# Optimization experiments

Hardware: AMD Instinct MI355X
Metric: run time of the kernel (lower is better)

The kernel has to match this reference:

```python
import jax, jax.numpy as jnp
import numpy as np
from jax import lax

B, H, W = 8, 512, 512


def setup_inputs() -> dict:
    key = jax.random.key(0)
    k1, k2, k3, k4, k5 = jax.random.split(key, 5)
    img = jax.random.uniform(k1, (B, 3, H, W), jnp.float32)
    omega = 0.8 + 0.15 * jax.random.uniform(k2, (B, 1), jnp.float32)
    atmospheric_light = 0.5 + 0.5 * jax.random.uniform(k3, (B, 3), jnp.float32)
    L_low = 2.0 * jax.random.uniform(k4, (B, 1), jnp.float32)          # percent in [0,2)
    L_high = 95.0 + 4.0 * jax.random.uniform(k5, (B, 1), jnp.float32)  # percent in [95,99)
    guided_radius = 15  # python int, uniform across batch (original clamps to [1,50])
    return {"img": img, "omega": omega, "atmospheric_light": atmospheric_light,
            "L_low": L_low, "L_high": L_high, "guided_radius": guided_radius}


def _box_filter(x, r):
    # reflect-pad + mean over (2r+1)x(2r+1) window, separable (exactly avg_pool2d on reflect-padded input)
    k = 2 * r + 1
    xp = jnp.pad(x, ((0, 0), (0, 0), (r, r), (r, r)), mode='reflect')
    s = lax.reduce_window(xp, 0.0, lax.add, (1, 1, k, 1), (1, 1, 1, 1), 'VALID')
    s = lax.reduce_window(s, 0.0, lax.add, (1, 1, 1, k), (1, 1, 1, 1), 'VALID')
    return s / (k * k)


def _forward(img, omega, atmospheric_light, L_low, L_high, r):
    eps = 0.5
    Bb, Cc, Hh, Ww = img.shape
    A = atmospheric_light.reshape(Bb, 3, 1, 1)
    # initial transmission: t = 1 - omega * min_c(I/A)
    dark = jnp.min(img / (A + 1e-8), axis=1, keepdims=True)           # (B,1,H,W)
    t0 = 1.0 - omega.reshape(Bb, 1, 1, 1) * dark
    # gradient constraint (weights from t0, applied to shifted copies)
    wx = jnp.exp(-jnp.abs(t0[:, :, :, 1:] - t0[:, :, :, :-1]))
    tx = jnp.concatenate([t0[:, :, :, :1], t0[:, :, :, :-1] * wx], axis=3)
    wy = jnp.exp(-jnp.abs(t0[:, :, 1:, :] - t0[:, :, :-1, :]))
    tg = jnp.concatenate([tx[:, :, :1, :], tx[:, :, :-1, :] * wy], axis=2)
    # guided filter with grayscale guide
    rgb_w = jnp.array([0.299, 0.587, 0.114], dtype=img.dtype).reshape(1, 3, 1, 1)
    gray = jnp.sum(img * rgb_w, axis=1, keepdims=True)                # (B,1,H,W)
    mI = _box_filter(gray, r)
    mp = _box_filter(tg, r)
    mIp = _box_filter(gray * tg, r)
    cov_Ip = mIp - mI * mp
    var_I = _box_filter(gray * gray, r) - mI * mI
    a = cov_Ip / (var_I + eps)
    b = mp - a * mI
    t_final = jnp.clip(_box_filter(a, r) * gray + _box_filter(b, r), 0.1, 1.0)
    # restoration
    J = jnp.clip((img - A) / (t_final + 1e-8) + A, 0.0, 1.0)
    # percentile color stretch (vectorized over B and C)
    n = Hh * Ww
    svals = jnp.sort(J.reshape(Bb, Cc, n), axis=-1)
    li = jnp.clip((L_low / 100.0 * n).astype(jnp.int32), 0, n - 1)    # (B,1)
    hi = jnp.clip((L_high / 100.0 * n).astype(jnp.int32), 0, n - 1)
    p_low = jnp.take_along_axis(svals, jnp.broadcast_to(li[:, :, None], (Bb, Cc, 1)), axis=-1).reshape(Bb, Cc, 1, 1)
    p_high = jnp.take_along_axis(svals, jnp.broadcast_to(hi[:, :, None], (Bb, Cc, 1)), axis=-1).reshape(Bb, Cc, 1, 1)
    out = (jnp.clip(J, p_low, p_high) - p_low) / (p_high - p_low + 1e-8)
    return jnp.clip(out, 0.0, 1.0)


def reference(img, omega, atmospheric_light, L_low, L_high, guided_radius):
    r = max(1, min(int(guided_radius), 50))
    return _forward(img, omega, atmospheric_light, L_low, L_high, r)
```

## Files before the change

kernel.cpp:

```cpp
#include <hip/hip_runtime.h>
#include <cstdint>

constexpr int Bb = 8, Hh = 512, Ww = 512;
constexpr int HWn = Hh * Ww;
constexpr int CH23 = 8;
constexpr int CHK4 = 16;
constexpr int NBIN = 1024;
constexpr int NSUB = 32;

__device__ __forceinline__ int reflect_idx(int p, int n) {
    p = (p < 0) ? -p : p;
    return (p < n) ? p : (2 * n - 2 - p);
}
__device__ __forceinline__ int clamp_r(const int* rad) {
    int r = rad[0];
    return (r < 1) ? 1 : ((r > 50) ? 50 : r);
}

__global__ __launch_bounds__(512) void k1_stats_h(
    const float* __restrict__ img, const float* __restrict__ omega,
    const float* __restrict__ atm, const int* __restrict__ rad,
    float4* __restrict__ hq, unsigned int* __restrict__ histzero)
{
    const int i = blockIdx.x;
    const int b = blockIdx.y;
    const int j = threadIdx.x;
    const int fbid = b * gridDim.x + i;
    if (fbid < 48) histzero[fbid * 512 + j] = 0u;
    const int r = clamp_r(rad);

    __shared__ float t0c[512], t0p[512];
    __shared__ float4 Pb[512];
    __shared__ float4 wsum[8];

    const float om = omega[b];
    const float iA0 = 1.0f / (atm[b*3+0] + 1e-8f);
    const float iA1 = 1.0f / (atm[b*3+1] + 1e-8f);
    const float iA2 = 1.0f / (atm[b*3+2] + 1e-8f);
    const float* imb = img + (size_t)b * 3 * HWn;
    const int ip = (i > 0) ? (i - 1) : 0;

    float r0 = imb[0*HWn + i*Ww + j];
    float g0 = imb[1*HWn + i*Ww + j];
    float b0 = imb[2*HWn + i*Ww + j];
    t0c[j] = 1.0f - om * fminf(fminf(r0*iA0, g0*iA1), b0*iA2);
    float r1 = imb[0*HWn + ip*Ww + j];
    float g1 = imb[1*HWn + ip*Ww + j];
    float b1 = imb[2*HWn + ip*Ww + j];
    t0p[j] = 1.0f - om * fminf(fminf(r1*iA0, g1*iA1), b1*iA2);
    float gr = 0.299f*r0 + 0.587f*g0 + 0.114f*b0;
    __syncthreads();

    float tx = (j == 0) ? t0p[0] : t0p[j-1] * __expf(-fabsf(t0p[j] - t0p[j-1]));
    float tgv = (i == 0) ? tx : tx * __expf(-fabsf(t0c[j] - t0p[j]));

    const int lane = j & 63, wv = j >> 6;
    float4 incl;
    incl.x = gr; incl.y = tgv; incl.z = gr * tgv; incl.w = gr * gr;
    #pragma unroll
    for (int off = 1; off < 64; off <<= 1) {
        float ux = __shfl_up(incl.x, off);
        float uy = __shfl_up(incl.y, off);
        float uz = __shfl_up(incl.z, off);
        float uw = __shfl_up(incl.w, off);
        if (lane >= off) { incl.x += ux; incl.y += uy; incl.z += uz; incl.w += uw; }
    }
    if (lane == 63) wsum[wv] = incl;
    __syncthreads();
    float4 o4; o4.x = 0.f; o4.y = 0.f; o4.z = 0.f; o4.w = 0.f;
    #pragma unroll
    for (int w = 0; w < 7; ++w) {
        if (w < wv) {
            float4 t = wsum[w];
            o4.x += t.x; o4.y += t.y; o4.z += t.z; o4.w += t.w;
        }
    }
    float4 P; P.x = incl.x + o4.x; P.y = incl.y + o4.y; P.z = incl.z + o4.z; P.w = incl.w + o4.w;
    Pb[j] = P;
    __syncthreads();

    const int lo = j - r, hi = j + r;
    float4 s = Pb[(hi > 511) ? 511 : hi];
    if (lo > 0) {
        float4 t = Pb[lo-1];
        s.x -= t.x; s.y -= t.y; s.z -= t.z; s.w -= t.w;
    }
    if (lo < 0) {
        float4 t = Pb[r - j], u = Pb[0];
        s.x += t.x - u.x; s.y += t.y - u.y; s.z += t.z - u.z; s.w += t.w - u.w;
    }
    if (hi > 511) {
        float4 t = Pb[510], u = Pb[1021 - j - r];
        s.x += t.x - u.x; s.y += t.y - u.y; s.z += t.z - u.z; s.w += t.w - u.w;
    }
    hq[((size_t)b * Hh + i) * Ww + j] = s;
}

__global__ __launch_bounds__(512) void k23_ab_h(
    const float4* __restrict__ hq, const int* __restrict__ rad,
    float2* __restrict__ hab)
{
    const int b  = blockIdx.y;
    const int y0 = blockIdx.x * CH23;
    const int j  = threadIdx.x;
    const int r  = clamp_r(rad);
    const float ikk = 1.0f / (float)((2*r+1) * (2*r+1));
    const int lane = j & 63, wv = j >> 6;

    __shared__ float2 Pb[512];
    __shared__ float2 wsum[8];

    float4 s; s.x = 0.f; s.y = 0.f; s.z = 0.f; s.w = 0.f;
    for (int d = -r; d <= r; ++d) {
        int m = reflect_idx(y0 + d, Hh);
        float4 v = hq[((size_t)b * Hh + m) * Ww + j];
        s.x += v.x; s.y += v.y; s.z += v.z; s.w += v.w;
    }

    for (int y = y0; y < y0 + CH23; ++y) {
        float mI = s.x * ikk, mp = s.y * ikk, mIp = s.z * ikk, mII = s.w * ikk;
        float av = (mIp - mI * mp) / (mII - mI * mI + 0.5f);
        float bv = mp - av * mI;

        float2 incl; incl.x = av; incl.y = bv;
        #pragma unroll
        for (int off = 1; off < 64; off <<= 1) {
            float ux = __shfl_up(incl.x, off);
            float uy = __shfl_up(incl.y, off);
            if (lane >= off) { incl.x += ux; incl.y += uy; }
        }
        if (lane == 63) wsum[wv] = incl;
        __syncthreads();
        float ox = 0.f, oy = 0.f;
        #pragma unroll
        for (int w = 0; w < 7; ++w) {
            if (w < wv) { float2 t = wsum[w]; ox += t.x; oy += t.y; }
        }
        float2 P; P.x = incl.x + ox; P.y = incl.y + oy;
        Pb[j] = P;
        __syncthreads();

        const int lo = j - r, hi = j + r;
        float2 hs = Pb[(hi > 511) ? 511 : hi];
        if (lo > 0)   { float2 t = Pb[lo-1];  hs.x -= t.x; hs.y -= t.y; }
        if (lo < 0)   { float2 t = Pb[r-j], u = Pb[0];
                        hs.x += t.x - u.x; hs.y += t.y - u.y; }
        if (hi > 511) { float2 t = Pb[510], u = Pb[1021-j-r];
                        hs.x += t.x - u.x; hs.y += t.y - u.y; }
        hab[((size_t)b * Hh + y) * Ww + j] = hs;

        int yin  = reflect_idx(y + 1 + r, Hh);
        int yout = reflect_idx(y - r, Hh);
        float4 vi = hq[((size_t)b * Hh + yin)  * Ww + j];
        float4 vo = hq[((size_t)b * Hh + yout) * Ww + j];
        s.x += vi.x - vo.x; s.y += vi.y - vo.y; s.z += vi.z - vo.z; s.w += vi.w - vo.w;
    }
}

__global__ __launch_bounds__(256) void k4_final_v(
    const float2* __restrict__ hab, const float* __restrict__ img,
    const float* __restrict__ atm, const int* __restrict__ rad,
    float* __restrict__ J)
{
    const int b  = blockIdx.y;
    const int y0 = blockIdx.x * CHK4;
    const int j  = blockIdx.z * 256 + threadIdx.x;
    const int r  = clamp_r(rad);
    const float ikk = 1.0f / (float)((2*r+1) * (2*r+1));

    float Aa[3];
    Aa[0] = atm[b*3+0]; Aa[1] = atm[b*3+1]; Aa[2] = atm[b*3+2];
    const float* imb = img + (size_t)b * 3 * HWn;
    float* Jb = J + (size_t)b * 3 * HWn;
    const float2* habb = hab + (size_t)b * Hh * Ww + j;

    float2 V; V.x = 0.f; V.y = 0.f;
    for (int d = -r; d <= r; ++d) {
        int m = reflect_idx(y0 + d, Hh);
        float2 v = habb[(size_t)m * Ww];
        V.x += v.x; V.y += v.y;
    }

    #pragma unroll
    for (int g = 0; g < CHK4; g += 4) {
        const int yb = y0 + g;
        float2 vi[4], vo[4];
        float cr[4], cg[4], cb[4];
        #pragma unroll
        for (int q = 0; q < 4; ++q) {
            const int y = yb + q;
            vi[q] = habb[(size_t)reflect_idx(y + 1 + r, Hh) * Ww];
            vo[q] = habb[(size_t)reflect_idx(y - r, Hh) * Ww];
            const size_t po = (size_t)y * Ww + j;
            cr[q] = imb[0*HWn + po];
            cg[q] = imb[1*HWn + po];
            cb[q] = imb[2*HWn + po];
        }
        #pragma unroll
        for (int q = 0; q < 4; ++q) {
            const int y = yb + q;
            const size_t po = (size_t)y * Ww + j;
            float g_ = 0.299f*cr[q] + 0.587f*cg[q] + 0.114f*cb[q];
            float t = fminf(fmaxf((V.x * g_ + V.y) * ikk, 0.1f), 1.0f);
            float invt = 1.0f / (t + 1e-8f);
            Jb[0*HWn + po] = fminf(fmaxf((cr[q] - Aa[0]) * invt + Aa[0], 0.f), 1.f);
            Jb[1*HWn + po] = fminf(fmaxf((cg[q] - Aa[1]) * invt + Aa[1], 0.f), 1.f);
            Jb[2*HWn + po] = fminf(fmaxf((cb[q] - Aa[2]) * invt + Aa[2], 0.f), 1.f);
            V.x += vi[q].x - vo[q].x;
            V.y += vi[q].y - vo[q].y;
        }
    }
}

__global__ __launch_bounds__(256) void k5_hist(
    const float4* __restrict__ J, unsigned int* __restrict__ hist)
{
    const int bc  = blockIdx.x >> 5;
    const int sub = blockIdx.x & (NSUB - 1);
    const int tid = threadIdx.x;
    __shared__ unsigned int lh[NBIN];
    for (int i = tid; i < NBIN; i += 256) lh[i] = 0u;
    __syncthreads();

    const float4* base = J + (size_t)bc * (HWn / 4) + (size_t)sub * (HWn / 4 / NSUB);
    unsigned int clo = 0, chi = 0;
    for (int i = tid; i < HWn / 4 / NSUB; i += 256) {
        float4 v = base[i];
        #pragma unroll
        for (int c = 0; c < 4; ++c) {
            float f = (c == 0) ? v.x : (c == 1) ? v.y : (c == 2) ? v.z : v.w;
            int bin = (int)(f * (float)NBIN);
            bin = (bin > NBIN-1) ? NBIN-1 : bin;
            if (bin == 0)           clo++;
            else if (bin == NBIN-1) chi++;
            else atomicAdd(&lh[bin], 1u);
        }
    }
    if (clo) atomicAdd(&lh[0], clo);
    if (chi) atomicAdd(&lh[NBIN-1], chi);
    __syncthreads();
    for (int i = tid; i < NBIN; i += 256) {
        unsigned int v = lh[i];
        if (v) atomicAdd(&hist[(size_t)bc * NBIN + i], v);
    }
}

__global__ __launch_bounds__(64) void k5_decide(
    const unsigned int* __restrict__ hist,
    const float* __restrict__ L_low, const float* __restrict__ L_high,
    float* __restrict__ p_low, float* __restrict__ p_high)
{
    const int t  = blockIdx.x / 24;
    const int bc = blockIdx.x % 24;
    const int b  = bc / 3;
    const int lane = threadIdx.x;
    const unsigned int* hb = hist + (size_t)bc * NBIN;

    unsigned int loc[NBIN / 64];
    unsigned int lsum = 0;
    #pragma unroll
    for (int i = 0; i < NBIN / 64; ++i) { loc[i] = hb[lane * (NBIN/64) + i]; lsum += loc[i]; }

    unsigned int incl = lsum;
    #pragma unroll
    for (int off = 1; off < 64; off <<= 1) {
        unsigned int v = __shfl_up(incl, off);
        if (lane >= off) incl += v;
    }
    unsigned int excl = incl - lsum;

    float L = t ? L_high[b] : L_low[b];
    int k = (int)(L * (1.0f / 100.0f) * (float)HWn);
    k = (k < 0) ? 0 : ((k > HWn - 1) ? HWn - 1 : k);

    if ((unsigned int)k >= excl && (unsigned int)k < incl) {
        unsigned int c = excl;
        #pragma unroll
        for (int i = 0; i < NBIN / 64; ++i) {
            if ((unsigned int)k < c + loc[i]) {
                float val = ((float)(lane * (NBIN/64) + i) + 0.5f) * (1.0f / (float)NBIN);
                if (t) p_high[bc] = val;
                else   p_low[bc]  = val;
                break;
            }
            c += loc[i];
        }
    }
}

__global__ __launch_bounds__(256) void k6_norm(
    float4* __restrict__ J,
    const float* __restrict__ p_low, const float* __restrict__ p_high)
{
    size_t idx = (size_t)blockIdx.x * 256 + threadIdx.x;
    int bc = (int)(idx >> 16);
    float l = p_low[bc], h = p_high[bc];
    float inv = 1.0f / (h - l + 1e-8f);
    float4 v = J[idx];
    v.x = fminf(fmaxf((fminf(fmaxf(v.x, l), h) - l) * inv, 0.f), 1.f);
    v.y = fminf(fmaxf((fminf(fmaxf(v.y, l), h) - l) * inv, 0.f), 1.f);
    v.z = fminf(fmaxf((fminf(fmaxf(v.z, l), h) - l) * inv, 0.f), 1.f);
    v.w = fminf(fmaxf((fminf(fmaxf(v.w, l), h) - l) * inv, 0.f), 1.f);
    J[idx] = v;
}

extern "C" void kernel_launch(void* const* d_in, const int* in_sizes, int n_in,
                              void* d_out, int out_size, void* d_ws, size_t ws_size,
                              hipStream_t stream)
{
    const float* img    = (const float*)d_in[0];
    const float* omega  = (const float*)d_in[1];
    const float* atm    = (const float*)d_in[2];
    const float* L_low  = (const float*)d_in[3];
    const float* L_high = (const float*)d_in[4];
    const int*   rad    = (const int*)d_in[5];
    float* J  = (float*)d_out;
    float* ws = (float*)d_ws;

    const size_t F = (size_t)Bb * HWn;
    float4* hq  = (float4*)ws;
    float2* hab = (float2*)(ws + 4 * F);
    unsigned int* hist = (unsigned int*)(ws + 6 * F);
    float* pl = (float*)(hist + 24 * NBIN);
    float* ph = pl + 32;

    k1_stats_h<<<dim3(Hh, Bb), 512, 0, stream>>>(img, omega, atm, rad, hq, hist);
    k23_ab_h  <<<dim3(Hh/CH23, Bb), 512, 0, stream>>>(hq, rad, hab);
    k4_final_v<<<dim3(Hh/CHK4, Bb, 2), 256, 0, stream>>>(hab, img, atm, rad, J);
    k5_hist   <<<24 * NSUB, 256, 0, stream>>>((const float4*)J, hist);
    k5_decide <<<48, 64, 0, stream>>>(hist, L_low, L_high, pl, ph);
    k6_norm   <<<(int)(3 * F / 4 / 256), 256, 0, stream>>>((float4*)J, pl, ph);
}
```

Measured before the change: 167.7 us.

## Fuse stats and a/b stages, box-filter vertically before horizontally

Merges the per-row statistics kernel and the a/b coefficient kernel into one. Each block recomputes the per-pixel guide statistics directly from the image with a vertical running sum over the window, then does the horizontal prefix-sum box filter for the stats and again for a/b. This drops the 4-float intermediate buffer and its global write/read, and one launch. In exchange each block recomputes stats rows for its halo (about 2r+1 extra rows per 16 output rows), does nine image loads per stats row, and keeps 16 float4 values in registers, which may cut occupancy.

```diff
diff --git a/kernel.cpp b/kernel.cpp
--- a/kernel.cpp
+++ b/kernel.cpp
@@ -3,7 +3,7 @@
 
 constexpr int Bb = 8, Hh = 512, Ww = 512;
 constexpr int HWn = Hh * Ww;
-constexpr int CH23 = 8;
+constexpr int CHF = 16;
 constexpr int CHK4 = 16;
 constexpr int NBIN = 1024;
 constexpr int NSUB = 32;
@@ -16,144 +16,182 @@
     int r = rad[0];
     return (r < 1) ? 1 : ((r > 50) ? 50 : r);
 }
-
-__global__ __launch_bounds__(512) void k1_stats_h(
+__device__ __forceinline__ void add4(float4& a, const float4& b) {
+    a.x += b.x; a.y += b.y; a.z += b.z; a.w += b.w;
+}
+__device__ __forceinline__ void sub4(float4& a, const float4& b) {
+    a.x -= b.x; a.y -= b.y; a.z -= b.z; a.w -= b.w;
+}
+
+__global__ __launch_bounds__(512) void k123_fused(
     const float* __restrict__ img, const float* __restrict__ omega,
     const float* __restrict__ atm, const int* __restrict__ rad,
-    float4* __restrict__ hq, unsigned int* __restrict__ histzero)
-{
-    const int i = blockIdx.x;
-    const int b = blockIdx.y;
-    const int j = threadIdx.x;
-    const int fbid = b * gridDim.x + i;
+    float2* __restrict__ hab, unsigned int* __restrict__ histzero)
+{
+    const int b  = blockIdx.y;
+    const int y0 = blockIdx.x * CHF;
+    const int j  = threadIdx.x;
+    const int fbid = b * gridDim.x + blockIdx.x;
     if (fbid < 48) histzero[fbid * 512 + j] = 0u;
     const int r = clamp_r(rad);
-
-    __shared__ float t0c[512], t0p[512];
-    __shared__ float4 Pb[512];
-    __shared__ float4 wsum[8];
-
-    const float om = omega[b];
+    const float ikk = 1.0f / (float)((2*r+1) * (2*r+1));
+    const int lane = j & 63, wv = j >> 6;
+    const int jm1 = (j > 0) ? j - 1 : 0;
+
+    __shared__ float4 P4[512];
+    __shared__ float2 P2[512];
+    __shared__ float4 w4s[8];
+    __shared__ float2 w2s[8];
+
+    const float om  = omega[b];
     const float iA0 = 1.0f / (atm[b*3+0] + 1e-8f);
     const float iA1 = 1.0f / (atm[b*3+1] + 1e-8f);
     const float iA2 = 1.0f / (atm[b*3+2] + 1e-8f);
     const float* imb = img + (size_t)b * 3 * HWn;
-    const int ip = (i > 0) ? (i - 1) : 0;
-
-    float r0 = imb[0*HWn + i*Ww + j];
-    float g0 = imb[1*HWn + i*Ww + j];
-    float b0 = imb[2*HWn + i*Ww + j];
-    t0c[j] = 1.0f - om * fminf(fminf(r0*iA0, g0*iA1), b0*iA2);
-    float r1 = imb[0*HWn + ip*Ww + j];
-    float g1 = imb[1*HWn + ip*Ww + j];
-    float b1 = imb[2*HWn + ip*Ww + j];
-    t0p[j] = 1.0f - om * fminf(fminf(r1*iA0, g1*iA1), b1*iA2);
-    float gr = 0.299f*r0 + 0.587f*g0 + 0.114f*b0;
-    __syncthreads();
-
-    float tx = (j == 0) ? t0p[0] : t0p[j-1] * __expf(-fabsf(t0p[j] - t0p[j-1]));
-    float tgv = (i == 0) ? tx : tx * __expf(-fabsf(t0c[j] - t0p[j]));
-
-    const int lane = j & 63, wv = j >> 6;
-    float4 incl;
-    incl.x = gr; incl.y = tgv; incl.z = gr * tgv; incl.w = gr * gr;
-    #pragma unroll
-    for (int off = 1; off < 64; off <<= 1) {
-        float ux = __shfl_up(incl.x, off);
-        float uy = __shfl_up(incl.y, off);
-        float uz = __shfl_up(incl.z, off);
-        float uw = __shfl_up(incl.w, off);
-        if (lane >= off) { incl.x += ux; incl.y += uy; incl.z += uz; incl.w += uw; }
-    }
-    if (lane == 63) wsum[wv] = incl;
-    __syncthreads();
-    float4 o4; o4.x = 0.f; o4.y = 0.f; o4.z = 0.f; o4.w = 0.f;
-    #pragma unroll
-    for (int w = 0; w < 7; ++w) {
-        if (w < wv) {
-            float4 t = wsum[w];
-            o4.x += t.x; o4.y += t.y; o4.z += t.z; o4.w += t.w;
-        }
-    }
-    float4 P; P.x = incl.x + o4.x; P.y = incl.y + o4.y; P.z = incl.z + o4.z; P.w = incl.w + o4.w;
-    Pb[j] = P;
-    __syncthreads();
+
+    auto stats_row = [&](int rr) -> float4 {
+        const int ip = (rr > 0) ? rr - 1 : 0;
+        float r0 = imb[0*HWn + rr*Ww + j];
+        float g0 = imb[1*HWn + rr*Ww + j];
+        float b0 = imb[2*HWn + rr*Ww + j];
+        float r1 = imb[0*HWn + ip*Ww + j];
+        float g1 = imb[1*HWn + ip*Ww + j];
+        float b1 = imb[2*HWn + ip*Ww + j];
+        float r2 = imb[0*HWn + ip*Ww + jm1];
+        float g2 = imb[1*HWn + ip*Ww + jm1];
+        float b2 = imb[2*HWn + ip*Ww + jm1];
+        float t0c  = 1.0f - om * fminf(fminf(r0*iA0, g0*iA1), b0*iA2);
+        float t0p  = 1.0f - om * fminf(fminf(r1*iA0, g1*iA1), b1*iA2);
+        float t0pm = 1.0f - om * fminf(fminf(r2*iA0, g2*iA1), b2*iA2);
+        float tx  = t0pm * __expf(-fabsf(t0p - t0pm));
+        float tgv = tx * __expf(-fabsf(t0c - t0p));
+        float gr  = 0.299f*r0 + 0.587f*g0 + 0.114f*b0;
+        float4 s; s.x = gr; s.y = tgv; s.z = gr * tgv; s.w = gr * gr;
+        return s;
+    };
+
+    float4 V; V.x = 0.f; V.y = 0.f; V.z = 0.f; V.w = 0.f;
+    for (int d = -r; d <= r; ++d) {
+        float4 s = stats_row(reflect_idx(y0 + d, Hh));
+        add4(V, s);
+    }
+    float4 v4r[CHF];
+    #pragma unroll
+    for (int k = 0; k < CHF; ++k) {
+        v4r[k] = V;
+        float4 si = stats_row(reflect_idx(y0 + k + 1 + r, Hh));
+        float4 so = stats_row(reflect_idx(y0 + k - r, Hh));
+        add4(V, si); sub4(V, so);
+    }
 
     const int lo = j - r, hi = j + r;
-    float4 s = Pb[(hi > 511) ? 511 : hi];
-    if (lo > 0) {
-        float4 t = Pb[lo-1];
-        s.x -= t.x; s.y -= t.y; s.z -= t.z; s.w -= t.w;
-    }
-    if (lo < 0) {
-        float4 t = Pb[r - j], u = Pb[0];
-        s.x += t.x - u.x; s.y += t.y - u.y; s.z += t.z - u.z; s.w += t.w - u.w;
-    }
-    if (hi > 511) {
-        float4 t = Pb[510], u = Pb[1021 - j - r];
-        s.x += t.x - u.x; s.y += t.y - u.y; s.z += t.z - u.z; s.w += t.w - u.w;
-    }
-    hq[((size_t)b * Hh + i) * Ww + j] = s;
-}
-
-__global__ __launch_bounds__(512) void k23_ab_h(
-    const float4* __restrict__ hq, const int* __restrict__ rad,
-    float2* __restrict__ hab)
-{
-    const int b  = blockIdx.y;
-    const int y0 = blockIdx.x * CH23;
-    const int j  = threadIdx.x;
-    const int r  = clamp_r(rad);
-    const float ikk = 1.0f / (float)((2*r+1) * (2*r+1));
-    const int lane = j & 63, wv = j >> 6;
-
-    __shared__ float2 Pb[512];
-    __shared__ float2 wsum[8];
-
-    float4 s; s.x = 0.f; s.y = 0.f; s.z = 0.f; s.w = 0.f;
-    for (int d = -r; d <= r; ++d) {
-        int m = reflect_idx(y0 + d, Hh);
-        float4 v = hq[((size_t)b * Hh + m) * Ww + j];
-        s.x += v.x; s.y += v.y; s.z += v.z; s.w += v.w;
-    }
-
-    for (int y = y0; y < y0 + CH23; ++y) {
-        float mI = s.x * ikk, mp = s.y * ikk, mIp = s.z * ikk, mII = s.w * ikk;
+    const int him = (hi > 511) ? 511 : hi;
+    const int pB = (lo > 0) ? (lo - 1) : 0;
+    const int pC = (lo < 0) ? (r - j) : 0;
+    const int pD = (hi > 511) ? (1021 - j - r) : 0;
+    const int iA_ = him >> 6, iB_ = pB >> 6, iC_ = pC >> 6, iD_ = pD >> 6;
+
+    #pragma unroll
+    for (int k = 0; k < CHF; ++k) {
+        float4 sc = v4r[k];
+        #pragma unroll
+        for (int off = 1; off < 64; off <<= 1) {
+            float ux = __shfl_up(sc.x, off);
+            float uy = __shfl_up(sc.y, off);
+            float uz = __shfl_up(sc.z, off);
+            float uw = __shfl_up(sc.w, off);
+            if (lane >= off) { sc.x += ux; sc.y += uy; sc.z += uz; sc.w += uw; }
+        }
+        P4[j] = sc;
+        if (lane == 63) w4s[wv] = sc;
+        __syncthreads();
+
+        float4 q0 = w4s[0], q1 = w4s[1], q2 = w4s[2], q3 = w4s[3];
+        float4 q4 = w4s[4], q5 = w4s[5], q6 = w4s[6];
+        #define WOFF4(idx, o)                                   \
+            { o.x=0.f;o.y=0.f;o.z=0.f;o.w=0.f;                  \
+              if ((idx) > 0) add4(o, q0);                       \
+              if ((idx) > 1) add4(o, q1);                       \
+              if ((idx) > 2) add4(o, q2);                       \
+              if ((idx) > 3) add4(o, q3);                       \
+              if ((idx) > 4) add4(o, q4);                       \
+              if ((idx) > 5) add4(o, q5);                       \
+              if ((idx) > 6) add4(o, q6); }
+        float4 oA; WOFF4(iA_, oA);
+        float4 s4 = P4[him]; add4(s4, oA);
+        if (lo > 0) {
+            float4 oB; WOFF4(iB_, oB);
+            float4 t = P4[pB]; add4(t, oB);
+            sub4(s4, t);
+        }
+        if (lo < 0) {
+            float4 oC; WOFF4(iC_, oC);
+            float4 t = P4[pC]; add4(t, oC);
+            float4 u = P4[0];
+            add4(s4, t); sub4(s4, u);
+        }
+        if (hi > 511) {
+            float4 t = P4[510];
+            float4 full; full.x=q0.x+q1.x+q2.x+q3.x+q4.x+q5.x+q6.x;
+            full.y=q0.y+q1.y+q2.y+q3.y+q4.y+q5.y+q6.y;
+            full.z=q0.z+q1.z+q2.z+q3.z+q4.z+q5.z+q6.z;
+            full.w=q0.w+q1.w+q2.w+q3.w+q4.w+q5.w+q6.w;
+            add4(t, full);
+            float4 oD; WOFF4(iD_, oD);
+            float4 u = P4[pD]; add4(u, oD);
+            add4(s4, t); sub4(s4, u);
+        }
+        #undef WOFF4
+
+        float mI = s4.x * ikk, mp = s4.y * ikk, mIp = s4.z * ikk, mII = s4.w * ikk;
         float av = (mIp - mI * mp) / (mII - mI * mI + 0.5f);
         float bv = mp - av * mI;
 
-        float2 incl; incl.x = av; incl.y = bv;
+        float sx = av, sy = bv;
         #pragma unroll
         for (int off = 1; off < 64; off <<= 1) {
-            float ux = __shfl_up(incl.x, off);
-            float uy = __shfl_up(incl.y, off);
-            if (lane >= off) { incl.x += ux; incl.y += uy; }
-        }
-        if (lane == 63) wsum[wv] = incl;
+            float ux = __shfl_up(sx, off);
+            float uy = __shfl_up(sy, off);
+            if (lane >= off) { sx += ux; sy += uy; }
+        }
+        P2[j].x = sx; P2[j].y = sy;
+        if (lane == 63) { w2s[wv].x = sx; w2s[wv].y = sy; }
         __syncthreads();
-        float ox = 0.f, oy = 0.f;
-        #pragma unroll
-        for (int w = 0; w < 7; ++w) {
-            if (w < wv) { float2 t = wsum[w]; ox += t.x; oy += t.y; }
-        }
-        float2 P; P.x = incl.x + ox; P.y = incl.y + oy;
-        Pb[j] = P;
-        __syncthreads();
-
-        const int lo = j - r, hi = j + r;
-        float2 hs = Pb[(hi > 511) ? 511 : hi];
-        if (lo > 0)   { float2 t = Pb[lo-1];  hs.x -= t.x; hs.y -= t.y; }
-        if (lo < 0)   { float2 t = Pb[r-j], u = Pb[0];
-                        hs.x += t.x - u.x; hs.y += t.y - u.y; }
-        if (hi > 511) { float2 t = Pb[510], u = Pb[1021-j-r];
-                        hs.x += t.x - u.x; hs.y += t.y - u.y; }
-        hab[((size_t)b * Hh + y) * Ww + j] = hs;
-
-        int yin  = reflect_idx(y + 1 + r, Hh);
-        int yout = reflect_idx(y - r, Hh);
-        float4 vi = hq[((size_t)b * Hh + yin)  * Ww + j];
-        float4 vo = hq[((size_t)b * Hh + yout) * Ww + j];
-        s.x += vi.x - vo.x; s.y += vi.y - vo.y; s.z += vi.z - vo.z; s.w += vi.w - vo.w;
+
+        float2 p0 = w2s[0], p1 = w2s[1], p2 = w2s[2], p3 = w2s[3];
+        float2 p4 = w2s[4], p5 = w2s[5], p6 = w2s[6];
+        #define WOFF2(idx, ox, oy)                              \
+            { ox = 0.f; oy = 0.f;                               \
+              if ((idx) > 0) { ox += p0.x; oy += p0.y; }        \
+              if ((idx) > 1) { ox += p1.x; oy += p1.y; }        \
+              if ((idx) > 2) { ox += p2.x; oy += p2.y; }        \
+              if ((idx) > 3) { ox += p3.x; oy += p3.y; }        \
+              if ((idx) > 4) { ox += p4.x; oy += p4.y; }        \
+              if ((idx) > 5) { ox += p5.x; oy += p5.y; }        \
+              if ((idx) > 6) { ox += p6.x; oy += p6.y; } }
+        float oxA, oyA; WOFF2(iA_, oxA, oyA);
+        float2 PA = P2[him];
+        float hsx = PA.x + oxA, hsy = PA.y + oyA;
+        if (lo > 0) {
+            float oxB, oyB; WOFF2(iB_, oxB, oyB);
+            float2 t = P2[pB];
+            hsx -= t.x + oxB; hsy -= t.y + oyB;
+        }
+        if (lo < 0) {
+            float oxC, oyC; WOFF2(iC_, oxC, oyC);
+            float2 t = P2[pC], u = P2[0];
+            hsx += (t.x + oxC) - u.x; hsy += (t.y + oyC) - u.y;
+        }
+        if (hi > 511) {
+            float fx = p0.x+p1.x+p2.x+p3.x+p4.x+p5.x+p6.x;
+            float fy = p0.y+p1.y+p2.y+p3.y+p4.y+p5.y+p6.y;
+            float oxD, oyD; WOFF2(iD_, oxD, oyD);
+            float2 t = P2[510], u = P2[pD];
+            hsx += (t.x + fx) - (u.x + oxD);
+            hsy += (t.y + fy) - (u.y + oyD);
+        }
+        #undef WOFF2
+        hab[((size_t)b * Hh + (y0 + k)) * Ww + j] = make_float2(hsx, hsy);
     }
 }
 
@@ -318,14 +356,12 @@
     float* ws = (float*)d_ws;
 
     const size_t F = (size_t)Bb * HWn;
-    float4* hq  = (float4*)ws;
-    float2* hab = (float2*)(ws + 4 * F);
-    unsigned int* hist = (unsigned int*)(ws + 6 * F);
+    float2* hab = (float2*)ws;
+    unsigned int* hist = (unsigned int*)(ws + 2 * F);
     float* pl = (float*)(hist + 24 * NBIN);
     float* ph = pl + 32;
 
-    k1_stats_h<<<dim3(Hh, Bb), 512, 0, stream>>>(img, omega, atm, rad, hq, hist);
-    k23_ab_h  <<<dim3(Hh/CH23, Bb), 512, 0, stream>>>(hq, rad, hab);
+    k123_fused<<<dim3(Hh/CHF, Bb), 512, 0, stream>>>(img, omega, atm, rad, hab, hist);
     k4_final_v<<<dim3(Hh/CHK4, Bb, 2), 256, 0, stream>>>(hab, img, atm, rad, J);
     k5_hist   <<<24 * NSUB, 256, 0, stream>>>((const float4*)J, hist);
     k5_decide <<<48, 64, 0, stream>>>(hist, L_low, L_high, pl, ph);
```

Result: slower. 198.6 us (+18.4%).
